# Optimization experiments

Measured on AMD Instinct MI355X. Metric: run time of the kernel, lower is better.

Reference implementation:

```python
import jax, jax.numpy as jnp
import numpy as np

H = 256   # hidden_size
IN = 2    # adding-problem input features
B, T = 128, 1024


def setup_inputs() -> dict:
    key = jax.random.key(0)
    ks = jax.random.split(key, 12)
    sc = 1.0 / np.sqrt(H)
    u = lambda k, shape: jax.random.uniform(k, shape, minval=-sc, maxval=sc, dtype=jnp.float32)
    return {
        "x": jax.random.normal(ks[0], (B, T, IN), dtype=jnp.float32),
        # GRU weights (torch layout: [3H, in], gate order r, z, n)
        "W_ih": u(ks[1], (3 * H, IN)),
        "W_hh": u(ks[2], (3 * H, H)),
        "b_ih": u(ks[3], (3 * H,)),
        "b_hh": u(ks[4], (3 * H,)),
        # adaptive momentum coefficient beta_t = sigmoid(x W + h U + b)
        "Wb_x": u(ks[5], (IN, 1)),
        "Wb_h": u(ks[6], (H, 1)),
        "b_beta": jnp.zeros((1,), dtype=jnp.float32),
        # momentum step size s (learnable scalar)
        "s": jnp.ones((), dtype=jnp.float32),
        # read-out head Linear(H, 1)
        "W_head": u(ks[7], (1, H)),
        "b_head": u(ks[8], (1,)),
    }


def reference(x, W_ih, W_hh, b_ih, b_hh, Wb_x, Wb_h, b_beta, s, W_head, b_head):
    Bm = x.shape[0]

    def step(carry, x_t):
        h, v = carry                                    # h: [B,H], v: [B,3H]
        beta = jax.nn.sigmoid(x_t @ Wb_x + h @ Wb_h + b_beta)   # [B,1]
        p = x_t @ W_ih.T + b_ih                         # input projection [B,3H]
        v = beta * v + s * p                            # momentum buffer
        gh = h @ W_hh.T + b_hh                          # hidden projection [B,3H]
        vr, vz, vn = jnp.split(v, 3, axis=-1)
        hr, hz, hn = jnp.split(gh, 3, axis=-1)
        r = jax.nn.sigmoid(vr + hr)
        z = jax.nn.sigmoid(vz + hz)
        n = jnp.tanh(vn + r * hn)
        h_new = (1.0 - z) * n + z * h
        return (h_new, v), beta[:, 0]

    h0 = jnp.zeros((Bm, H), dtype=x.dtype)
    v0 = jnp.zeros((Bm, 3 * H), dtype=x.dtype)
    (hT, _), betas = jax.lax.scan(step, (h0, v0), jnp.transpose(x, (1, 0, 2)))
    out = hT @ W_head.T + b_head                        # head on last timestep, [B,1]
    return (out, betas.T)                               # betas: [B,T]
```

## Files before the change

kernel.cpp:

```cpp
#include <hip/hip_runtime.h>

#define HID 256
#define TLEN 1024
#define BATCH 128

typedef _Float16 half2_t __attribute__((ext_vector_type(2)));

__device__ __forceinline__ float fexp2(float x) { return __builtin_amdgcn_exp2f(x); }
__device__ __forceinline__ float frcp(float x)  { return __builtin_amdgcn_rcpf(x); }
__device__ __forceinline__ float fast_sigmoid(float x) {
  return frcp(1.0f + fexp2(-1.442695040888963f * x));
}
__device__ __forceinline__ float fast_tanh(float x) {
  float e = fexp2(2.885390081777927f * x);
  return 1.0f - 2.0f * frcp(e + 1.0f);
}
__device__ __forceinline__ float dot2acc(half2_t a, half2_t b, float c) {
  return __builtin_amdgcn_fdot2(a, b, c, false);
}

#if defined(__has_builtin) && __has_builtin(__builtin_amdgcn_sdot4)
#define SDOT4(a, b, c) __builtin_amdgcn_sdot4((int)(a), (int)(b), (c), false)
#else
__device__ __forceinline__ int SDOT4(int a, int b, int c) {
#pragma unroll
  for (int e = 0; e < 4; ++e)
    c += ((a << (24 - 8 * e)) >> 24) * ((b << (24 - 8 * e)) >> 24);
  return c;
}
#endif

#define DPP_ADD_F(var, ctrl, rmask)                                            \
  var += __builtin_bit_cast(float, __builtin_amdgcn_update_dpp(                \
      0, __builtin_bit_cast(int, var), (ctrl), (rmask), 0xf, true))
#define DPP_ADD_I(var, ctrl, rmask)                                            \
  var += __builtin_amdgcn_update_dpp(0, (var), (ctrl), (rmask), 0xf, true)

__device__ __forceinline__ float wave_sum63_f(float p) {
  DPP_ADD_F(p, 0x111, 0xf);
  DPP_ADD_F(p, 0x112, 0xf);
  DPP_ADD_F(p, 0x114, 0xf);
  DPP_ADD_F(p, 0x118, 0xf);
  DPP_ADD_F(p, 0x142, 0xa);
  DPP_ADD_F(p, 0x143, 0xc);
  return p;
}
__device__ __forceinline__ int wave_sum63_i(int p) {
  DPP_ADD_I(p, 0x111, 0xf);
  DPP_ADD_I(p, 0x112, 0xf);
  DPP_ADD_I(p, 0x114, 0xf);
  DPP_ADD_I(p, 0x118, 0xf);
  DPP_ADD_I(p, 0x142, 0xa);
  DPP_ADD_I(p, 0x143, 0xc);
  return p;
}

__global__ void quant_whh(const float* __restrict__ W_hh,
                          const float* __restrict__ Wb_h,
                          uint4* __restrict__ wq,
                          float* __restrict__ scales,
                          unsigned* __restrict__ wbq,
                          float* __restrict__ wbscale) {
  const int r = blockIdx.x * 256 + threadIdx.x;
  if (r < 768) {
    const float* row = W_hh + (size_t)r * HID;
    float amax = 0.0f;
    for (int k = 0; k < HID; ++k) amax = fmaxf(amax, fabsf(row[k]));
    amax = fmaxf(amax, 1e-20f);
    scales[r] = amax / 127.0f;
    const float inv = 127.0f / amax;
    const int g = r >> 8, dd = r & 255;
    for (int c = 0; c < 16; ++c) {
      unsigned w[4];
#pragma unroll
      for (int u = 0; u < 4; ++u) {
        unsigned bb = 0;
#pragma unroll
        for (int e = 0; e < 4; ++e) {
          int qv = (int)rintf(row[16 * c + 4 * u + e] * inv);
          bb |= (unsigned)(qv & 0xff) << (8 * e);
        }
        w[u] = bb;
      }
      wq[(size_t)dd * 48 + g * 16 + c] = uint4{w[0], w[1], w[2], w[3]};
    }
  } else if (r < 832) {
    float amax = 0.0f;
    for (int k = 0; k < HID; ++k) amax = fmaxf(amax, fabsf(Wb_h[k]));
    amax = fmaxf(amax, 1e-20f);
    const float inv = 127.0f / amax;
    const int i = r - 768;
    unsigned bb = 0;
#pragma unroll
    for (int e = 0; e < 4; ++e) {
      int qv = (int)rintf(Wb_h[4 * i + e] * inv);
      bb |= (unsigned)(qv & 0xff) << (8 * e);
    }
    wbq[i] = bb;
    if (i == 0) wbscale[0] = (amax / 127.0f) * (1.0f / 127.0f);
  }
}

__global__
__attribute__((amdgpu_flat_work_group_size(256, 256)))
__attribute__((amdgpu_waves_per_eu(1, 1)))
void momgru_persistent(const float* __restrict__ x,
                       const float* __restrict__ W_ih,
                       const float* __restrict__ b_ih,
                       const float* __restrict__ b_hh,
                       const float* __restrict__ Wb_x,
                       const float* __restrict__ b_beta,
                       const float* __restrict__ s_ptr,
                       const float* __restrict__ W_head,
                       const float* __restrict__ b_head,
                       const uint4* __restrict__ wq,
                       const float* __restrict__ scales,
                       const unsigned* __restrict__ wbq,
                       const float* __restrict__ wbscale,
                       float* __restrict__ out)
{
  const int b    = blockIdx.x;
  const int tid  = threadIdx.x;
  const int lane = tid & 63;
  const int wv   = tid >> 6;

  __shared__ unsigned hq[2][64];
  __shared__ float    red[4];

  const uint4* wqt = wq + (size_t)tid * 48;
  uint4 wr[16], wz[16], wn[16];
#pragma unroll
  for (int j = 0; j < 16; ++j) wr[j] = wqt[j];
#pragma unroll
  for (int j = 0; j < 16; ++j) wz[j] = wqt[16 + j];
#pragma unroll
  for (int j = 0; j < 16; ++j) wn[j] = wqt[32 + j];

  const float sv = s_ptr[0];
  const half2_t wih_r = half2_t{(_Float16)(sv * W_ih[2 * tid]),             (_Float16)(sv * W_ih[2 * tid + 1])};
  const half2_t wih_z = half2_t{(_Float16)(sv * W_ih[2 * (HID + tid)]),     (_Float16)(sv * W_ih[2 * (HID + tid) + 1])};
  const half2_t wih_n = half2_t{(_Float16)(sv * W_ih[2 * (2 * HID + tid)]), (_Float16)(sv * W_ih[2 * (2 * HID + tid) + 1])};
  const float bih_r = sv * b_ih[tid], bih_z = sv * b_ih[HID + tid], bih_n = sv * b_ih[2 * HID + tid];
  const float bhh_r = b_hh[tid], bhh_z = b_hh[HID + tid], bhh_n = b_hh[2 * HID + tid];
  const float sc_r = scales[tid] * (1.0f / 127.0f);
  const float sc_z = scales[HID + tid] * (1.0f / 127.0f);
  const float sc_n = scales[2 * HID + tid] * (1.0f / 127.0f);
  const half2_t wbx2 = half2_t{(_Float16)Wb_x[0], (_Float16)Wb_x[1]};
  const float bbeta = b_beta[0];
  const unsigned wbq_l = wbq[lane];
  const float wbsc = wbscale[0];

  if (tid < 128) reinterpret_cast<unsigned*>(hq)[tid] = 0u;
  if (tid < 4) red[tid] = 0.0f;
  float h_old = 0.0f, vr = 0.0f, vz = 0.0f, vn = 0.0f;
  float* betas = out + BATCH;
  const float2* xg2 = reinterpret_cast<const float2*>(x + (size_t)b * TLEN * 2);
  float2 xv = xg2[0];
  __syncthreads();

  int cur = 0;
  for (int t = 0; t < TLEN; ++t) {
    const unsigned hw_l = reinterpret_cast<const unsigned*>(hq[cur])[lane];
    int hwb_i = SDOT4(hw_l, wbq_l, 0);
    hwb_i = wave_sum63_i(hwb_i);

    int ar0 = 0, az0 = 0, an0 = 0, ar1 = 0, az1 = 0, an1 = 0;
    const int4* hb = reinterpret_cast<const int4*>(hq[cur]);
#pragma unroll
    for (int c = 0; c < 8; ++c) {
      const int4 h0 = hb[2 * c];
      const int4 h1 = hb[2 * c + 1];
      ar0 = SDOT4(h0.x, wr[2 * c].x, ar0);
      az0 = SDOT4(h0.x, wz[2 * c].x, az0);
      an0 = SDOT4(h0.x, wn[2 * c].x, an0);
      ar1 = SDOT4(h1.x, wr[2 * c + 1].x, ar1);
      az1 = SDOT4(h1.x, wz[2 * c + 1].x, az1);
      an1 = SDOT4(h1.x, wn[2 * c + 1].x, an1);
      ar0 = SDOT4(h0.y, wr[2 * c].y, ar0);
      az0 = SDOT4(h0.y, wz[2 * c].y, az0);
      an0 = SDOT4(h0.y, wn[2 * c].y, an0);
      ar1 = SDOT4(h1.y, wr[2 * c + 1].y, ar1);
      az1 = SDOT4(h1.y, wz[2 * c + 1].y, az1);
      an1 = SDOT4(h1.y, wn[2 * c + 1].y, an1);
      ar0 = SDOT4(h0.z, wr[2 * c].z, ar0);
      az0 = SDOT4(h0.z, wz[2 * c].z, az0);
      an0 = SDOT4(h0.z, wn[2 * c].z, an0);
      ar1 = SDOT4(h1.z, wr[2 * c + 1].z, ar1);
      az1 = SDOT4(h1.z, wz[2 * c + 1].z, az1);
      an1 = SDOT4(h1.z, wn[2 * c + 1].z, an1);
      ar0 = SDOT4(h0.w, wr[2 * c].w, ar0);
      az0 = SDOT4(h0.w, wz[2 * c].w, az0);
      an0 = SDOT4(h0.w, wn[2 * c].w, an0);
      ar1 = SDOT4(h1.w, wr[2 * c + 1].w, ar1);
      az1 = SDOT4(h1.w, wz[2 * c + 1].w, az1);
      an1 = SDOT4(h1.w, wn[2 * c + 1].w, an1);
    }
    const int ar = ar0 + ar1, az = az0 + az1, an = an0 + an1;

    const float hWb = (float)__builtin_amdgcn_readlane(hwb_i, 63) * wbsc;
    const half2_t x2 = half2_t{(_Float16)xv.x, (_Float16)xv.y};
    xv = xg2[(t + 1 < TLEN) ? t + 1 : t];
    const float beta = fast_sigmoid(dot2acc(x2, wbx2, hWb + bbeta));
    vr = beta * vr + dot2acc(x2, wih_r, bih_r);
    vz = beta * vz + dot2acc(x2, wih_z, bih_z);
    vn = beta * vn + dot2acc(x2, wih_n, bih_n);

    const float r = fast_sigmoid(vr + (float)ar * sc_r + bhh_r);
    const float z = fast_sigmoid(vz + (float)az * sc_z + bhh_z);
    const float n = fast_tanh(vn + r * ((float)an * sc_n + bhh_n));
    h_old = (1.0f - z) * n + z * h_old;

    const int nxt = cur ^ 1;
    const int qb = (int)rintf(h_old * 127.0f);
    reinterpret_cast<unsigned char*>(hq[nxt])[tid] = (unsigned char)(qb & 0xff);

    if (tid == 0) betas[(size_t)b * TLEN + t] = beta;

    __syncthreads();
    cur = nxt;
  }

  float hp = h_old * W_head[tid];
  hp = wave_sum63_f(hp);
  if (lane == 63) red[wv] = hp;
  __syncthreads();
  if (tid == 0) out[b] = red[0] + red[1] + red[2] + red[3] + b_head[0];
}

extern "C" void kernel_launch(void* const* d_in, const int* in_sizes, int n_in,
                              void* d_out, int out_size, void* d_ws, size_t ws_size,
                              hipStream_t stream) {
  const float* x      = (const float*)d_in[0];
  const float* W_ih   = (const float*)d_in[1];
  const float* W_hh   = (const float*)d_in[2];
  const float* b_ih   = (const float*)d_in[3];
  const float* b_hh   = (const float*)d_in[4];
  const float* Wb_x   = (const float*)d_in[5];
  const float* Wb_h   = (const float*)d_in[6];
  const float* b_beta = (const float*)d_in[7];
  const float* s      = (const float*)d_in[8];
  const float* W_head = (const float*)d_in[9];
  const float* b_head = (const float*)d_in[10];
  float* out = (float*)d_out;

  char* wsb = (char*)d_ws;
  uint4*    wq      = (uint4*)wsb;
  float*    scales  = (float*)(wsb + 196608);
  unsigned* wbq     = (unsigned*)(wsb + 199680);
  float*    wbscale = (float*)(wsb + 199936);

  quant_whh<<<dim3(4), dim3(256), 0, stream>>>(W_hh, Wb_h, wq, scales, wbq, wbscale);
  momgru_persistent<<<dim3(BATCH), dim3(256), 0, stream>>>(
      x, W_ih, b_ih, b_hh, Wb_x, b_beta, s, W_head, b_head,
      (const uint4*)wq, (const float*)scales, (const unsigned*)wbq,
      (const float*)wbscale, out);
}
```

Measured before the change: 824.9 us.

## Compute recurrent hidden projection with int8 MFMA instead of sdot4

Replaces the per-thread sdot4 dot products for h·W_hh with int8 16x16x32 MFMA instructions. Weights are prepacked by a new pack_a kernel into the MFMA A-operand layout, and h is fed as a B operand with only one valid column. Results go through shared memory with an extra barrier. This trades scalar dot-product issue for matrix-unit throughput, but most of each MFMA's columns do no useful work, and it adds an LDS round trip and a barrier per timestep.

```diff
diff --git a/kernel.cpp b/kernel.cpp
--- a/kernel.cpp
+++ b/kernel.cpp
@@ -5,6 +5,15 @@
 #define BATCH 128
 
 typedef _Float16 half2_t __attribute__((ext_vector_type(2)));
+typedef int i32x4 __attribute__((ext_vector_type(4)));
+
+#if defined(__HIP_DEVICE_COMPILE__)
+#if !__has_builtin(__builtin_amdgcn_mfma_i32_16x16x32_i8)
+#error "mfma_i32_16x16x32_i8 builtin missing on gfx950 device pass"
+#endif
+#endif
+
+#define SDOT4(a, b, c) __builtin_amdgcn_sdot4((int)(a), (int)(b), (c), false)
 
 __device__ __forceinline__ float fexp2(float x) { return __builtin_amdgcn_exp2f(x); }
 __device__ __forceinline__ float frcp(float x)  { return __builtin_amdgcn_rcpf(x); }
@@ -18,17 +27,6 @@
 __device__ __forceinline__ float dot2acc(half2_t a, half2_t b, float c) {
   return __builtin_amdgcn_fdot2(a, b, c, false);
 }
-
-#if defined(__has_builtin) && __has_builtin(__builtin_amdgcn_sdot4)
-#define SDOT4(a, b, c) __builtin_amdgcn_sdot4((int)(a), (int)(b), (c), false)
-#else
-__device__ __forceinline__ int SDOT4(int a, int b, int c) {
-#pragma unroll
-  for (int e = 0; e < 4; ++e)
-    c += ((a << (24 - 8 * e)) >> 24) * ((b << (24 - 8 * e)) >> 24);
-  return c;
-}
-#endif
 
 #define DPP_ADD_F(var, ctrl, rmask)                                            \
   var += __builtin_bit_cast(float, __builtin_amdgcn_update_dpp(                \
@@ -55,35 +53,17 @@
   return p;
 }
 
-__global__ void quant_whh(const float* __restrict__ W_hh,
-                          const float* __restrict__ Wb_h,
-                          uint4* __restrict__ wq,
-                          float* __restrict__ scales,
-                          unsigned* __restrict__ wbq,
-                          float* __restrict__ wbscale) {
+__global__ void prep_scales(const float* __restrict__ W_hh,
+                            const float* __restrict__ Wb_h,
+                            float* __restrict__ scales,
+                            unsigned* __restrict__ wbq,
+                            float* __restrict__ wbscale) {
   const int r = blockIdx.x * 256 + threadIdx.x;
   if (r < 768) {
     const float* row = W_hh + (size_t)r * HID;
     float amax = 0.0f;
     for (int k = 0; k < HID; ++k) amax = fmaxf(amax, fabsf(row[k]));
-    amax = fmaxf(amax, 1e-20f);
-    scales[r] = amax / 127.0f;
-    const float inv = 127.0f / amax;
-    const int g = r >> 8, dd = r & 255;
-    for (int c = 0; c < 16; ++c) {
-      unsigned w[4];
-#pragma unroll
-      for (int u = 0; u < 4; ++u) {
-        unsigned bb = 0;
-#pragma unroll
-        for (int e = 0; e < 4; ++e) {
-          int qv = (int)rintf(row[16 * c + 4 * u + e] * inv);
-          bb |= (unsigned)(qv & 0xff) << (8 * e);
-        }
-        w[u] = bb;
-      }
-      wq[(size_t)dd * 48 + g * 16 + c] = uint4{w[0], w[1], w[2], w[3]};
-    }
+    scales[r] = fmaxf(amax, 1e-20f) / 127.0f;
   } else if (r < 832) {
     float amax = 0.0f;
     for (int k = 0; k < HID; ++k) amax = fmaxf(amax, fabsf(Wb_h[k]));
@@ -99,6 +79,34 @@
     wbq[i] = bb;
     if (i == 0) wbscale[0] = (amax / 127.0f) * (1.0f / 127.0f);
   }
+}
+
+__global__ void pack_a(const float* __restrict__ W_hh,
+                       const float* __restrict__ scales,
+                       unsigned long long* __restrict__ aq) {
+  const int idx = blockIdx.x * 256 + threadIdx.x;
+  const int w = idx / 6144;
+  const int rem = idx - w * 6144;
+  const int i = rem >> 6;
+  const int l = rem & 63;
+  const int rt = i >> 3, s = i & 7;
+  const int g = rt >> 2, jb = rt & 3;
+  const int row = 256 * g + 64 * w + 16 * jb + (l & 15);
+  const int k0 = 32 * s + 8 * (l >> 4);
+  const float inv = frcp(scales[row]);
+  const float* rp = W_hh + (size_t)row * HID + k0;
+  unsigned lo = 0, hi = 0;
+#pragma unroll
+  for (int e = 0; e < 4; ++e) {
+    int qv = (int)rintf(rp[e] * inv);
+    lo |= (unsigned)(qv & 0xff) << (8 * e);
+  }
+#pragma unroll
+  for (int e = 0; e < 4; ++e) {
+    int qv = (int)rintf(rp[4 + e] * inv);
+    hi |= (unsigned)(qv & 0xff) << (8 * e);
+  }
+  aq[idx] = ((unsigned long long)hi << 32) | lo;
 }
 
 __global__
@@ -113,7 +121,7 @@
                        const float* __restrict__ s_ptr,
                        const float* __restrict__ W_head,
                        const float* __restrict__ b_head,
-                       const uint4* __restrict__ wq,
+                       const unsigned long long* __restrict__ aq,
                        const float* __restrict__ scales,
                        const unsigned* __restrict__ wbq,
                        const float* __restrict__ wbscale,
@@ -125,16 +133,13 @@
   const int wv   = tid >> 6;
 
   __shared__ unsigned hq[2][64];
+  __shared__ int      gd[4 * 192];
   __shared__ float    red[4];
 
-  const uint4* wqt = wq + (size_t)tid * 48;
-  uint4 wr[16], wz[16], wn[16];
-#pragma unroll
-  for (int j = 0; j < 16; ++j) wr[j] = wqt[j];
-#pragma unroll
-  for (int j = 0; j < 16; ++j) wz[j] = wqt[16 + j];
-#pragma unroll
-  for (int j = 0; j < 16; ++j) wn[j] = wqt[32 + j];
+  long long wa[96];
+#pragma unroll
+  for (int i = 0; i < 96; ++i)
+    wa[i] = (long long)aq[(size_t)(wv * 96 + i) * 64 + lane];
 
   const float sv = s_ptr[0];
   const half2_t wih_r = half2_t{(_Float16)(sv * W_ih[2 * tid]),             (_Float16)(sv * W_ih[2 * tid + 1])};
@@ -156,6 +161,8 @@
   float* betas = out + BATCH;
   const float2* xg2 = reinterpret_cast<const float2*>(x + (size_t)b * TLEN * 2);
   float2 xv = xg2[0];
+  const bool bact = (lane & 15) == 0;
+  const int  boff = (lane >> 4) * 8;
   __syncthreads();
 
   int cur = 0;
@@ -164,38 +171,37 @@
     int hwb_i = SDOT4(hw_l, wbq_l, 0);
     hwb_i = wave_sum63_i(hwb_i);
 
-    int ar0 = 0, az0 = 0, an0 = 0, ar1 = 0, az1 = 0, an1 = 0;
-    const int4* hb = reinterpret_cast<const int4*>(hq[cur]);
-#pragma unroll
-    for (int c = 0; c < 8; ++c) {
-      const int4 h0 = hb[2 * c];
-      const int4 h1 = hb[2 * c + 1];
-      ar0 = SDOT4(h0.x, wr[2 * c].x, ar0);
-      az0 = SDOT4(h0.x, wz[2 * c].x, az0);
-      an0 = SDOT4(h0.x, wn[2 * c].x, an0);
-      ar1 = SDOT4(h1.x, wr[2 * c + 1].x, ar1);
-      az1 = SDOT4(h1.x, wz[2 * c + 1].x, az1);
-      an1 = SDOT4(h1.x, wn[2 * c + 1].x, an1);
-      ar0 = SDOT4(h0.y, wr[2 * c].y, ar0);
-      az0 = SDOT4(h0.y, wz[2 * c].y, az0);
-      an0 = SDOT4(h0.y, wn[2 * c].y, an0);
-      ar1 = SDOT4(h1.y, wr[2 * c + 1].y, ar1);
-      az1 = SDOT4(h1.y, wz[2 * c + 1].y, az1);
-      an1 = SDOT4(h1.y, wn[2 * c + 1].y, an1);
-      ar0 = SDOT4(h0.z, wr[2 * c].z, ar0);
-      az0 = SDOT4(h0.z, wz[2 * c].z, az0);
-      an0 = SDOT4(h0.z, wn[2 * c].z, an0);
-      ar1 = SDOT4(h1.z, wr[2 * c + 1].z, ar1);
-      az1 = SDOT4(h1.z, wz[2 * c + 1].z, az1);
-      an1 = SDOT4(h1.z, wn[2 * c + 1].z, an1);
-      ar0 = SDOT4(h0.w, wr[2 * c].w, ar0);
-      az0 = SDOT4(h0.w, wz[2 * c].w, az0);
-      an0 = SDOT4(h0.w, wn[2 * c].w, an0);
-      ar1 = SDOT4(h1.w, wr[2 * c + 1].w, ar1);
-      az1 = SDOT4(h1.w, wz[2 * c + 1].w, az1);
-      an1 = SDOT4(h1.w, wn[2 * c + 1].w, an1);
-    }
-    const int ar = ar0 + ar1, az = az0 + az1, an = an0 + an1;
+    const char* hbytes = reinterpret_cast<const char*>(hq[cur]);
+    long long B[8];
+#pragma unroll
+    for (int s = 0; s < 8; ++s) {
+      long long v = 0;
+      if (bact) v = *reinterpret_cast<const long long*>(hbytes + 32 * s + boff);
+      B[s] = v;
+    }
+
+    i32x4 acc[12];
+#pragma unroll
+    for (int rt = 0; rt < 12; ++rt) {
+      i32x4 c = {0, 0, 0, 0};
+#pragma unroll
+      for (int s = 0; s < 8; ++s)
+        c = __builtin_amdgcn_mfma_i32_16x16x32_i8(wa[rt * 8 + s], B[s], c, 0, 0, 0);
+      acc[rt] = c;
+    }
+
+    if (bact) {
+      const int q4 = (lane >> 4) * 4;
+#pragma unroll
+      for (int rt = 0; rt < 12; ++rt) {
+        const int g = rt >> 2, jb = rt & 3;
+        *reinterpret_cast<i32x4*>(&gd[wv * 192 + g * 64 + jb * 16 + q4]) = acc[rt];
+      }
+    }
+    __syncthreads();
+    const int ar = gd[wv * 192 + lane];
+    const int az = gd[wv * 192 + 64 + lane];
+    const int an = gd[wv * 192 + 128 + lane];
 
     const float hWb = (float)__builtin_amdgcn_readlane(hwb_i, 63) * wbsc;
     const half2_t x2 = half2_t{(_Float16)xv.x, (_Float16)xv.y};
@@ -244,14 +250,15 @@
   float* out = (float*)d_out;
 
   char* wsb = (char*)d_ws;
-  uint4*    wq      = (uint4*)wsb;
+  unsigned long long* aq = (unsigned long long*)wsb;
   float*    scales  = (float*)(wsb + 196608);
   unsigned* wbq     = (unsigned*)(wsb + 199680);
   float*    wbscale = (float*)(wsb + 199936);
 
-  quant_whh<<<dim3(4), dim3(256), 0, stream>>>(W_hh, Wb_h, wq, scales, wbq, wbscale);
+  prep_scales<<<dim3(4), dim3(256), 0, stream>>>(W_hh, Wb_h, scales, wbq, wbscale);
+  pack_a<<<dim3(96), dim3(256), 0, stream>>>(W_hh, scales, aq);
   momgru_persistent<<<dim3(BATCH), dim3(256), 0, stream>>>(
       x, W_ih, b_ih, b_hh, Wb_x, b_beta, s, W_head, b_head,
-      (const uint4*)wq, (const float*)scales, (const unsigned*)wbq,
-      (const float*)wbscale, out);
-}
+      (const unsigned long long*)aq, (const float*)scales,
+      (const unsigned*)wbq, (const float*)wbscale, out);
+}
```

Result: slower. 1.443 ms (+74.9%).
